# Optimization experiments

Measured on AMD Instinct MI355X. Metric: run time of the kernel, lower is better.

Reference implementation:

```python
import jax, jax.numpy as jnp
import numpy as np

RBF_RADIUS = 12.0
NUM_GAUSSIANS = 50
NUM_ELEMENTS = 100
NUM_MASKS = 1
NUM_HEADS = 8
N_NODES = 50000
N_EDGES = 1000000


def setup_inputs() -> dict:
    key = jax.random.key(0)
    k1, k2, k3, k4 = jax.random.split(key, 4)
    anum = jax.random.randint(k1, (N_NODES,), 0, NUM_ELEMENTS)
    edge_index = jax.random.randint(k2, (2, N_EDGES), 0, N_NODES)
    dist = jax.random.uniform(k3, (N_EDGES,), dtype=jnp.float32) * RBF_RADIUS
    embedding = jax.random.normal(
        k4, (NUM_ELEMENTS, NUM_ELEMENTS, NUM_MASKS, NUM_HEADS, NUM_GAUSSIANS),
        dtype=jnp.float32)
    return {"anum": anum, "edge_index": edge_index, "dist": dist,
            "embedding": embedding}


def _gaussian_smearing(dist):
    # offsets evenly spaced on [0, rbf_radius], std = rbf_radius / num_gaussians
    offsets = jnp.linspace(0.0, RBF_RADIUS, NUM_GAUSSIANS, dtype=jnp.float32)
    std = RBF_RADIUS / NUM_GAUSSIANS
    coeff = -0.5 / (std * std)
    diff = dist[:, None] - offsets[None, :]          # [E, G]
    return jnp.exp(coeff * diff * diff)              # [E, G]


def reference(anum, edge_index, dist, embedding):
    rbf = _gaussian_smearing(dist)                   # [E, G]
    src = anum[edge_index[0]]                        # [E]
    dst = anum[edge_index[1]]                        # [E]
    alphas = embedding[src, dst]                     # [E, M, H, G]
    # einsum 'ijkl,il->jik': i=edges, j=masks, k=heads, l=gaussians
    attn_bias = jnp.einsum('emhg,eg->meh', alphas, rbf)  # [M, E, H]
    return attn_bias
```

## Files before the change

kernel.cpp:

```cpp
#include <hip/hip_runtime.h>


#define G_NUM 50
#define H_NUM 8
#define NE_NUM 100
#define N_PAIRS (NE_NUM * NE_NUM)
#define WIN 8
#define BLOCK_THREADS 256
#define TP_PAIRS 8

#define SPACING (12.0f / (float)(G_NUM - 1))
#define INV_SPACING ((float)(G_NUM - 1) / 12.0f)
#define RBF_COEFF (-0.5f * ((float)G_NUM / 12.0f) * ((float)G_NUM / 12.0f))

__device__ __forceinline__ float bf_lo(unsigned u) { return __uint_as_float(u << 16); }
__device__ __forceinline__ float bf_hi(unsigned u) { return __uint_as_float(u & 0xffff0000u); }

__global__ __launch_bounds__(BLOCK_THREADS) void transpose_cast_kernel(
    const float* __restrict__ emb, unsigned int* __restrict__ temb)
{
    __shared__ float ls[TP_PAIRS * H_NUM * G_NUM];

    const int tid = threadIdx.x;
    const int p0  = blockIdx.x * TP_PAIRS;

    const float4* src = (const float4*)(emb + (size_t)p0 * (H_NUM * G_NUM));
    #pragma unroll
    for (int i = tid; i < TP_PAIRS * H_NUM * G_NUM / 4; i += BLOCK_THREADS)
        ((float4*)ls)[i] = src[i];
    __syncthreads();

    unsigned int* dst = temb + (size_t)p0 * (H_NUM * G_NUM / 2);
    #pragma unroll
    for (int i = tid; i < TP_PAIRS * H_NUM * G_NUM / 2; i += BLOCK_THREADS) {
        int q  = i / (H_NUM * G_NUM / 2);
        int u  = i - q * (H_NUM * G_NUM / 2);
        int g  = u >> 2;
        int h0 = (u & 3) * 2;
        float f0 = ls[q * (H_NUM * G_NUM) + h0 * G_NUM + g];
        float f1 = ls[q * (H_NUM * G_NUM) + (h0 + 1) * G_NUM + g];
        unsigned u0 = __float_as_uint(f0);
        unsigned u1 = __float_as_uint(f1);
        unsigned b0 = (u0 + 0x7fffu + ((u0 >> 16) & 1u)) >> 16;
        unsigned b1 = (u1 + 0x7fffu + ((u1 >> 16) & 1u)) >> 16;
        dst[i] = (b1 << 16) | (b0 & 0xffffu);
    }
}

__global__ __launch_bounds__(BLOCK_THREADS) void gather_kernel(
    const int* __restrict__ anum,
    const int* __restrict__ edge_index,
    const float* __restrict__ dist,
    const unsigned short* __restrict__ temb,
    float* __restrict__ out,
    int n_edges)
{
    int e = blockIdx.x * BLOCK_THREADS + threadIdx.x;
    if (e >= n_edges) return;

    int s = edge_index[e];
    int d = edge_index[n_edges + e];
    int p = anum[s] * NE_NUM + anum[d];
    float dv = dist[e];

    int g0 = (int)(dv * INV_SPACING) - 3;
    if (g0 < 0) g0 = 0;
    if (g0 > G_NUM - WIN) g0 = G_NUM - WIN;

    const unsigned short* wb = temb + (size_t)p * (H_NUM * G_NUM) + g0 * H_NUM;

    uint4 v[WIN];
    #pragma unroll
    for (int r = 0; r < WIN; ++r)
        v[r] = *(const uint4*)(wb + r * H_NUM);

    float a0 = 0.f, a1 = 0.f, a2 = 0.f, a3 = 0.f;
    float a4 = 0.f, a5 = 0.f, a6 = 0.f, a7 = 0.f;
    #pragma unroll
    for (int r = 0; r < WIN; ++r) {
        float diff = dv - (float)(g0 + r) * SPACING;
        float rb = __expf(RBF_COEFF * diff * diff);
        a0 += rb * bf_lo(v[r].x);
        a1 += rb * bf_hi(v[r].x);
        a2 += rb * bf_lo(v[r].y);
        a3 += rb * bf_hi(v[r].y);
        a4 += rb * bf_lo(v[r].z);
        a5 += rb * bf_hi(v[r].z);
        a6 += rb * bf_lo(v[r].w);
        a7 += rb * bf_hi(v[r].w);
    }

    float* ob = out + (size_t)e * H_NUM;
    *(float4*)(ob)     = make_float4(a0, a1, a2, a3);
    *(float4*)(ob + 4) = make_float4(a4, a5, a6, a7);
}

__global__ __launch_bounds__(BLOCK_THREADS) void direct_kernel(
    const int* __restrict__ anum,
    const int* __restrict__ edge_index,
    const float* __restrict__ dist,
    const float* __restrict__ emb,
    float* __restrict__ out,
    int n_edges)
{
    __shared__ int   pair_s[32];
    __shared__ float dist_sd[32];
    __shared__ float rbf_sd[32 * G_NUM];

    const int tid = threadIdx.x;
    const int e0  = blockIdx.x * 32;

    if (tid < 32) {
        int e = e0 + tid;
        if (e >= n_edges) e = n_edges - 1;
        int s  = edge_index[e];
        int d  = edge_index[n_edges + e];
        pair_s[tid] = (anum[s] * NE_NUM + anum[d]) * (H_NUM * G_NUM);
        dist_sd[tid] = dist[e];
    }
    __syncthreads();

    for (int idx = tid; idx < 32 * G_NUM; idx += BLOCK_THREADS) {
        int el = idx / G_NUM;
        int g  = idx - el * G_NUM;
        float diff = dist_sd[el] - (float)g * SPACING;
        rbf_sd[idx] = __expf(RBF_COEFF * diff * diff);
    }
    __syncthreads();

    const int el = tid >> 3;
    const int h  = tid & 7;
    const float* ebase = emb + pair_s[el] + h * G_NUM;
    const float* rbase = rbf_sd + el * G_NUM;

    float acc = 0.0f;
    #pragma unroll
    for (int g2 = 0; g2 < G_NUM / 2; ++g2) {
        float2 ev = *(const float2*)(ebase + 2 * g2);
        float2 rv = *(const float2*)(rbase + 2 * g2);
        acc += ev.x * rv.x + ev.y * rv.y;
    }

    if (e0 + el < n_edges)
        out[e0 * H_NUM + tid] = acc;
}

extern "C" void kernel_launch(void* const* d_in, const int* in_sizes, int n_in,
                              void* d_out, int out_size, void* d_ws, size_t ws_size,
                              hipStream_t stream) {
    const int*   anum       = (const int*)d_in[0];
    const int*   edge_index = (const int*)d_in[1];
    const float* dist       = (const float*)d_in[2];
    const float* emb        = (const float*)d_in[3];
    float*       out        = (float*)d_out;
    const int n_edges = in_sizes[2];

    const size_t temb_bytes = (size_t)N_PAIRS * H_NUM * G_NUM * sizeof(unsigned short);

    if (ws_size < temb_bytes) {
        const int grid = (n_edges + 31) / 32;
        direct_kernel<<<grid, BLOCK_THREADS, 0, stream>>>(
            anum, edge_index, dist, emb, out, n_edges);
        return;
    }

    unsigned int* temb = (unsigned int*)d_ws;

    transpose_cast_kernel<<<N_PAIRS / TP_PAIRS, BLOCK_THREADS, 0, stream>>>(emb, temb);

    const int grid = (n_edges + BLOCK_THREADS - 1) / BLOCK_THREADS;
    gather_kernel<<<grid, BLOCK_THREADS, 0, stream>>>(
        anum, edge_index, dist, (const unsigned short*)temb, out, n_edges);
}
```

Before: 114.8 us.

## Cooperative 8-lane gather per edge with swizzle butterfly reduction in gather kernel

Restructures gather_kernel so each group of 8 lanes processes one edge, with each lane loading one 16-byte row of the 8-gaussian window. This replaces one thread issuing eight scattered 16-byte loads. Partial products are reduced across lanes using ds_swizzle butterfly steps, which leaves each lane holding the sum for one head. Output stores become fully coalesced, and edge_index, dist and out use nontemporal loads and stores. The cost is extra swizzle and select instructions, plus an LDS staging step for per-edge offsets.

```diff
diff --git a/kernel.cpp b/kernel.cpp
--- a/kernel.cpp
+++ b/kernel.cpp
@@ -7,6 +7,7 @@
 #define N_PAIRS (NE_NUM * NE_NUM)
 #define WIN 8
 #define BLOCK_THREADS 256
+#define WAVES_PB (BLOCK_THREADS / 64)
 #define TP_PAIRS 8
 
 #define SPACING (12.0f / (float)(G_NUM - 1))
@@ -15,6 +16,11 @@
 
 __device__ __forceinline__ float bf_lo(unsigned u) { return __uint_as_float(u << 16); }
 __device__ __forceinline__ float bf_hi(unsigned u) { return __uint_as_float(u & 0xffff0000u); }
+
+#define SWZ(x, pat) __int_as_float(__builtin_amdgcn_ds_swizzle(__float_as_int(x), (pat)))
+#define SWZ_X1 0x041F
+#define SWZ_X2 0x081F
+#define SWZ_X4 0x101F
 
 __global__ __launch_bounds__(BLOCK_THREADS) void transpose_cast_kernel(
     const float* __restrict__ emb, unsigned int* __restrict__ temb)
@@ -55,44 +61,69 @@
     float* __restrict__ out,
     int n_edges)
 {
-    int e = blockIdx.x * BLOCK_THREADS + threadIdx.x;
-    if (e >= n_edges) return;
-
-    int s = edge_index[e];
-    int d = edge_index[n_edges + e];
-    int p = anum[s] * NE_NUM + anum[d];
-    float dv = dist[e];
-
-    int g0 = (int)(dv * INV_SPACING) - 3;
-    if (g0 < 0) g0 = 0;
-    if (g0 > G_NUM - WIN) g0 = G_NUM - WIN;
-
-    const unsigned short* wb = temb + (size_t)p * (H_NUM * G_NUM) + g0 * H_NUM;
-
-    uint4 v[WIN];
-    #pragma unroll
-    for (int r = 0; r < WIN; ++r)
-        v[r] = *(const uint4*)(wb + r * H_NUM);
-
-    float a0 = 0.f, a1 = 0.f, a2 = 0.f, a3 = 0.f;
-    float a4 = 0.f, a5 = 0.f, a6 = 0.f, a7 = 0.f;
-    #pragma unroll
-    for (int r = 0; r < WIN; ++r) {
-        float diff = dv - (float)(g0 + r) * SPACING;
+    __shared__ int   m_off[BLOCK_THREADS];
+    __shared__ float m_res[BLOCK_THREADS];
+
+    const int tid  = threadIdx.x;
+    const int lane = tid & 63;
+    const int wv   = tid >> 6;
+    const int row  = lane & 7;
+    const int grp  = lane >> 3;
+
+    const int we0 = (blockIdx.x * WAVES_PB + wv) * 64;
+
+    {
+        int e  = we0 + lane;
+        int ec = e < n_edges ? e : (n_edges - 1);
+        int s  = __builtin_nontemporal_load(edge_index + ec);
+        int d  = __builtin_nontemporal_load(edge_index + n_edges + ec);
+        float dv = __builtin_nontemporal_load(dist + ec);
+        int p  = anum[s] * NE_NUM + anum[d];
+        int g0 = (int)(dv * INV_SPACING) - 3;
+        g0 = g0 < 0 ? 0 : g0;
+        g0 = g0 > (G_NUM - WIN) ? (G_NUM - WIN) : g0;
+        m_off[tid] = p * (G_NUM * H_NUM) + g0 * H_NUM;
+        m_res[tid] = dv - (float)g0 * SPACING;
+    }
+
+    const int base = wv * 64;
+    uint4 vv[8];
+    float rs[8];
+    #pragma unroll
+    for (int t = 0; t < 8; ++t) {
+        int off = m_off[base + t * 8 + grp];
+        rs[t]   = m_res[base + t * 8 + grp];
+        const unsigned short* wb = temb + (size_t)(unsigned)off + row * H_NUM;
+        vv[t] = *(const uint4*)wb;
+    }
+
+    const float rowsp = (float)row * SPACING;
+    const bool b0 = (row & 1) != 0;
+    const bool b1 = (row & 2) != 0;
+    const bool b2 = (row & 4) != 0;
+    float* ob = out + (size_t)we0 * H_NUM + lane;
+
+    #pragma unroll
+    for (int t = 0; t < 8; ++t) {
+        float diff = rs[t] - rowsp;
         float rb = __expf(RBF_COEFF * diff * diff);
-        a0 += rb * bf_lo(v[r].x);
-        a1 += rb * bf_hi(v[r].x);
-        a2 += rb * bf_lo(v[r].y);
-        a3 += rb * bf_hi(v[r].y);
-        a4 += rb * bf_lo(v[r].z);
-        a5 += rb * bf_hi(v[r].z);
-        a6 += rb * bf_lo(v[r].w);
-        a7 += rb * bf_hi(v[r].w);
-    }
-
-    float* ob = out + (size_t)e * H_NUM;
-    *(float4*)(ob)     = make_float4(a0, a1, a2, a3);
-    *(float4*)(ob + 4) = make_float4(a4, a5, a6, a7);
+        uint4 v = vv[t];
+        float a0 = rb * bf_lo(v.x), a1 = rb * bf_hi(v.x);
+        float a2 = rb * bf_lo(v.y), a3 = rb * bf_hi(v.y);
+        float a4 = rb * bf_lo(v.z), a5 = rb * bf_hi(v.z);
+        float a6 = rb * bf_lo(v.w), a7 = rb * bf_hi(v.w);
+
+        float k0 = (b0 ? a1 : a0) + SWZ(b0 ? a0 : a1, SWZ_X1);
+        float k1 = (b0 ? a3 : a2) + SWZ(b0 ? a2 : a3, SWZ_X1);
+        float k2 = (b0 ? a5 : a4) + SWZ(b0 ? a4 : a5, SWZ_X1);
+        float k3 = (b0 ? a7 : a6) + SWZ(b0 ? a6 : a7, SWZ_X1);
+        float c0 = (b1 ? k1 : k0) + SWZ(b1 ? k0 : k1, SWZ_X2);
+        float c1 = (b1 ? k3 : k2) + SWZ(b1 ? k2 : k3, SWZ_X2);
+        float r8 = (b2 ? c1 : c0) + SWZ(b2 ? c0 : c1, SWZ_X4);
+
+        if (we0 + t * 8 + grp < n_edges)
+            __builtin_nontemporal_store(r8, ob + t * 64);
+    }
 }
 
 __global__ __launch_bounds__(BLOCK_THREADS) void direct_kernel(
```

Result: no change. 115.3 us (+0.4%).
